# Optimization experiments

Measured on AMD Instinct MI355X. Metric: run time of the kernel, lower is better.

Reference implementation:

```python
import jax, jax.numpy as jnp
import numpy as np

D_IN = 1024
D_OUT = 1024


def setup_inputs() -> dict:
    key = jax.random.key(0)
    ks = jax.random.split(key, 7)
    x = jax.random.normal(ks[0], (4, 2048, D_IN), dtype=jnp.float32)
    scale = 1.0 / np.sqrt(D_IN)
    Wq = jax.random.normal(ks[1], (D_IN, D_OUT), dtype=jnp.float32) * scale
    Wk = jax.random.normal(ks[2], (D_IN, D_OUT), dtype=jnp.float32) * scale
    Wv = jax.random.normal(ks[3], (D_IN, D_OUT), dtype=jnp.float32) * scale
    bq = jax.random.normal(ks[4], (D_OUT,), dtype=jnp.float32) * 0.01
    bk = jax.random.normal(ks[5], (D_OUT,), dtype=jnp.float32) * 0.01
    bv = jax.random.normal(ks[6], (D_OUT,), dtype=jnp.float32) * 0.01
    return {"x": x, "Wq": Wq, "bq": bq, "Wk": Wk, "bk": bk, "Wv": Wv, "bv": bv}


def reference(x, Wq, bq, Wk, bk, Wv, bv):
    # x: [B, S, d_in]
    q = jnp.einsum("bsd,de->bse", x, Wq) + bq  # [B, S, d_out]
    k = jnp.einsum("bsd,de->bse", x, Wk) + bk
    v = jnp.einsum("bsd,de->bse", x, Wv) + bv
    d_out = q.shape[-1]
    scores = jnp.einsum("bqe,bke->bqk", q, k) / jnp.sqrt(jnp.float32(d_out))
    attn = jax.nn.softmax(scores, axis=-1)  # [B, S, S]
    return jnp.einsum("bqk,bke->bqe", attn, v)
```

## Files before the change

### kernel.cpp

```cpp
#include <hip/hip_runtime.h>
#include <hip/hip_bf16.h>
#include <stdint.h>

typedef __bf16 bf16x8 __attribute__((ext_vector_type(8)));
typedef __bf16 bf16x4 __attribute__((ext_vector_type(4)));
typedef float f32x4 __attribute__((ext_vector_type(4)));

#define DEV __device__ __forceinline__

DEV void gload_lds16(const void* g, void* l) {
  __builtin_amdgcn_global_load_lds((const __attribute__((address_space(1))) void*)g,
                                   (__attribute__((address_space(3))) void*)l, 16, 0, 0);
}

#define WAITV0 asm volatile("s_waitcnt vmcnt(0)" ::: "memory")
#define MFMA16x16(a, b, c) __builtin_amdgcn_mfma_f32_16x16x32_bf16(a, b, c, 0, 0, 0)

__global__ __launch_bounds__(256) void pack_x_kernel(const float* __restrict__ x,
                                                     __bf16* __restrict__ o, long n) {
  long i = ((long)blockIdx.x * 256 + threadIdx.x) * 4;
  const long stride = (long)gridDim.x * 256 * 4;
  for (; i < n; i += stride) {
    f32x4 v = *(const f32x4*)(x + i);
    bf16x4 b;
    b[0] = (__bf16)v[0]; b[1] = (__bf16)v[1]; b[2] = (__bf16)v[2]; b[3] = (__bf16)v[3];
    *(bf16x4*)(o + i) = b;
  }
}

__global__ __launch_bounds__(256) void pack_w_kernel(const float* __restrict__ Wq,
                                                     const float* __restrict__ Wk,
                                                     const float* __restrict__ Wv,
                                                     __bf16* __restrict__ Wt) {
  const int w = blockIdx.z;
  const float* W = (w == 0) ? Wq : (w == 1) ? Wk : Wv;
  const float scale = (w == 0) ? 0.03125f : 1.0f;
  const int d0 = blockIdx.x * 64;
  const int e0 = blockIdx.y * 64;
  __shared__ __bf16 T[64][72];
  const int tid = threadIdx.x;
  const int r4 = tid >> 4;
  const int c4 = (tid & 15) * 4;
#pragma unroll
  for (int p = 0; p < 4; ++p) {
    int r = r4 + p * 16;
    f32x4 v = *(const f32x4*)(W + (long)(d0 + r) * 1024 + e0 + c4);
    T[r][c4 + 0] = (__bf16)(v[0] * scale);
    T[r][c4 + 1] = (__bf16)(v[1] * scale);
    T[r][c4 + 2] = (__bf16)(v[2] * scale);
    T[r][c4 + 3] = (__bf16)(v[3] * scale);
  }
  __syncthreads();
  const int e4 = tid >> 3;
  const int dd = (tid & 7) * 8;
#pragma unroll
  for (int p = 0; p < 2; ++p) {
    int e = e4 + p * 32;
    bf16x8 ov;
#pragma unroll
    for (int j = 0; j < 8; ++j) ov[j] = T[dd + j][e];
    *(bf16x8*)(Wt + (long)w * 1048576 + (long)(e0 + e) * 1024 + d0 + dd) = ov;
  }
}

__global__ __launch_bounds__(256) void pack_bias_kernel(const float* __restrict__ bq,
                                                        const float* __restrict__ bk,
                                                        const float* __restrict__ bv,
                                                        float* __restrict__ o) {
  int i = blockIdx.x * 256 + threadIdx.x;
  if (i < 1024) o[i] = bq[i] * 0.03125f;
  else if (i < 2048) o[i] = bk[i - 1024];
  else if (i < 3072) o[i] = bv[i - 2048];
}

template <int MODE>
__global__ __launch_bounds__(256, 2) void gemm128_kernel(
    const __bf16* __restrict__ A, int lda,
    const __bf16* __restrict__ B, int ldb, long long bBatchStride, int bmShift,
    const float* __restrict__ bias,
    void* __restrict__ C, int ldc,
    __bf16* __restrict__ vt,
    int nTiles, int nt) {
  constexpr int TILEB = 16384;
  __shared__ __attribute__((aligned(128))) char lds[2 * 2 * TILEB];

  const int tid = threadIdx.x;
  const int lane = tid & 63;
  const int wid = tid >> 6;
  const int wm = wid >> 1, wn = wid & 1;
  const int lo = lane & 15, hi = lane >> 4;

  const int cpx = gridDim.x >> 3;
  const int bid = blockIdx.x;
  const int swz = (bid & 7) * cpx + (bid >> 3);
  const int bm = swz / nTiles, bn = swz % nTiles;

  const __bf16* Bb = B + (long long)(bm >> bmShift) * bBatchStride;

  const __bf16* gA[4]; const __bf16* gB[4]; int lA[4];
#pragma unroll
  for (int l = 0; l < 4; ++l) {
    int s = l * 256 + tid, r = s >> 3;
    int c = (s & 7) ^ (r & 7);
    gA[l] = A + (long long)(bm * 128 + r) * lda + c * 8;
    gB[l] = Bb + (long long)(bn * 128 + r) * ldb + c * 8;
    lA[l] = s * 16;
  }

  const int c0 = ((0 * 4 + hi) ^ (lo & 7)) << 4;
  const int c1 = ((1 * 4 + hi) ^ (lo & 7)) << 4;
  const int aBase = (wm * 64 + lo) * 128;
  const int bBase = TILEB + (wn * 64 + lo) * 128;

  f32x4 acc[4][4] = {};

#define STAGE(tt, buf)                                                \
  do {                                                                \
    const long long ko_ = (long long)(tt) * 64;                       \
    char* lb_ = lds + (buf) * (2 * TILEB);                            \
    _Pragma("unroll") for (int l = 0; l < 4; ++l) {                   \
      gload_lds16(gA[l] + ko_, lb_ + lA[l]);                          \
      gload_lds16(gB[l] + ko_, lb_ + TILEB + lA[l]);                  \
    }                                                                 \
  } while (0)

  STAGE(0, 0);
  WAITV0;
  __builtin_amdgcn_s_barrier();
  __builtin_amdgcn_sched_barrier(0);

  for (int t = 0; t < nt; ++t) {
    if (t + 1 < nt) STAGE(t + 1, (t + 1) & 1);
    const char* base = lds + (t & 1) * (2 * TILEB);

    bf16x8 av[4][2], bv[4][2];
#pragma unroll
    for (int f = 0; f < 4; ++f) {
      av[f][0] = *(const bf16x8*)(base + aBase + f * 16 * 128 + c0);
      av[f][1] = *(const bf16x8*)(base + aBase + f * 16 * 128 + c1);
      bv[f][0] = *(const bf16x8*)(base + bBase + f * 16 * 128 + c0);
      bv[f][1] = *(const bf16x8*)(base + bBase + f * 16 * 128 + c1);
    }
#pragma unroll
    for (int mi = 0; mi < 4; ++mi)
#pragma unroll
      for (int ni = 0; ni < 4; ++ni) {
        acc[mi][ni] = MFMA16x16(av[mi][0], bv[ni][0], acc[mi][ni]);
        acc[mi][ni] = MFMA16x16(av[mi][1], bv[ni][1], acc[mi][ni]);
      }

    if (t + 1 < nt) {
      WAITV0;
      __builtin_amdgcn_s_barrier();
      __builtin_amdgcn_sched_barrier(0);
    }
  }
#undef STAGE

  const long long row0 = (long long)bm * 128 + wm * 64 + hi * 4;
  const long long col0 = (long long)bn * 128 + wn * 64 + lo;

  if (MODE == 0) {
    float* Cf = (float*)C;
#pragma unroll
    for (int ni = 0; ni < 4; ++ni) {
      const long long col = col0 + ni * 16;
#pragma unroll
      for (int mi = 0; mi < 4; ++mi)
#pragma unroll
        for (int j = 0; j < 4; ++j)
          Cf[(row0 + mi * 16 + j) * ldc + col] = acc[mi][ni][j];
    }
  } else if (MODE == 1) {
    __bf16* Ch = (__bf16*)C;
#pragma unroll
    for (int ni = 0; ni < 4; ++ni) {
      const long long col = col0 + ni * 16;
#pragma unroll
      for (int mi = 0; mi < 4; ++mi)
#pragma unroll
        for (int j = 0; j < 4; ++j)
          Ch[(row0 + mi * 16 + j) * ldc + col] = (__bf16)acc[mi][ni][j];
    }
  } else {
    if (bn < 16) {
      __bf16* Ch = (__bf16*)C;
#pragma unroll
      for (int ni = 0; ni < 4; ++ni) {
        const long long col = col0 + ni * 16;
        const float bvs = bias[col];
#pragma unroll
        for (int mi = 0; mi < 4; ++mi)
#pragma unroll
          for (int j = 0; j < 4; ++j)
            Ch[(row0 + mi * 16 + j) * ldc + col] = (__bf16)(acc[mi][ni][j] + bvs);
      }
    } else {
      const int b = bm >> 4;
      __bf16* vtb = vt + (long long)b * 2097152;
      const int t0 = (bm & 15) * 128 + wm * 64 + hi * 4;
#pragma unroll
      for (int ni = 0; ni < 4; ++ni) {
        const long long e = (long long)(bn - 16) * 128 + wn * 64 + ni * 16 + lo;
        const float bvs = bias[2048 + e];
#pragma unroll
        for (int mi = 0; mi < 4; ++mi) {
          bf16x4 o;
#pragma unroll
          for (int j = 0; j < 4; ++j) o[j] = (__bf16)(acc[mi][ni][j] + bvs);
          *(bf16x4*)(vtb + e * 2048 + t0 + mi * 16) = o;
        }
      }
    }
  }
}

__global__ __launch_bounds__(256) void softmax_kernel(__bf16* __restrict__ S) {
  const long long row = blockIdx.x;
  __bf16* p = S + row * 2048;
  const int tid = threadIdx.x;
  const int lane = tid & 63, wid = tid >> 6;
  bf16x8 v = *(const bf16x8*)(p + tid * 8);
  float xv[8];
#pragma unroll
  for (int j = 0; j < 8; ++j) xv[j] = (float)v[j];
  float mx = xv[0];
#pragma unroll
  for (int j = 1; j < 8; ++j) mx = fmaxf(mx, xv[j]);
#pragma unroll
  for (int off = 32; off >= 1; off >>= 1) mx = fmaxf(mx, __shfl_xor(mx, off));
  __shared__ float red[8];
  if (lane == 0) red[wid] = mx;
  __syncthreads();
  mx = fmaxf(fmaxf(red[0], red[1]), fmaxf(red[2], red[3]));
  float e[8];
  float sum = 0.f;
#pragma unroll
  for (int j = 0; j < 8; ++j) {
    e[j] = __expf(xv[j] - mx);
    sum += e[j];
  }
#pragma unroll
  for (int off = 32; off >= 1; off >>= 1) sum += __shfl_xor(sum, off);
  if (lane == 0) red[4 + wid] = sum;
  __syncthreads();
  sum = red[4] + red[5] + red[6] + red[7];
  const float inv = 1.0f / sum;
  bf16x8 ov;
#pragma unroll
  for (int j = 0; j < 8; ++j) ov[j] = (__bf16)(e[j] * inv);
  *(bf16x8*)(p + tid * 8) = ov;
}

extern "C" void kernel_launch(void* const* d_in, const int* in_sizes, int n_in,
                              void* d_out, int out_size, void* d_ws, size_t ws_size,
                              hipStream_t stream) {
  (void)in_sizes; (void)n_in; (void)out_size;
  const float* x  = (const float*)d_in[0];
  const float* Wq = (const float*)d_in[1];
  const float* bq = (const float*)d_in[2];
  const float* Wk = (const float*)d_in[3];
  const float* bk = (const float*)d_in[4];
  const float* Wv = (const float*)d_in[5];
  const float* bv = (const float*)d_in[6];
  float* out = (float*)d_out;
  char* ws = (char*)d_ws;
  if (ws_size < 124000000ULL) return;

  __bf16* x16  = (__bf16*)(ws + 0);
  __bf16* Wt   = (__bf16*)(ws + 16777216);
  float*  bqkv = (float*)(ws + 23068672);
  __bf16* QKV  = (__bf16*)(ws + 23080960);
  __bf16* Vt   = (__bf16*)(ws + 73412608);
  __bf16* S    = (__bf16*)(ws + 90189824);

  pack_x_kernel<<<2048, 256, 0, stream>>>(x, x16, 8388608L);
  pack_w_kernel<<<dim3(16, 16, 3), 256, 0, stream>>>(Wq, Wk, Wv, Wt);
  pack_bias_kernel<<<12, 256, 0, stream>>>(bq, bk, bv, bqkv);

  gemm128_kernel<2><<<dim3(1536), 256, 0, stream>>>(
      x16, 1024, Wt, 1024, 0LL, 30, bqkv, QKV, 3072, Vt, 24, 16);

  gemm128_kernel<1><<<dim3(1024), 256, 0, stream>>>(
      QKV, 3072, QKV + 1024, 3072, 6291456LL, 4, nullptr, S, 2048, nullptr, 16, 16);

  softmax_kernel<<<8192, 256, 0, stream>>>(S);

  gemm128_kernel<0><<<dim3(512), 256, 0, stream>>>(
      S, 2048, Vt, 2048, 2097152LL, 4, nullptr, out, 1024, nullptr, 8, 32);
}
```

Before: 166.9 us.

## Fuse softmax exp into QK GEMM epilogue and defer normalization to PV GEMM

Replaces the standalone softmax pass with exp computed in the QK^T GEMM epilogue, which also writes per-tile partial row sums. A small rowsum kernel turns these into reciprocals, and the PV GEMM scales its output rows by them. The QKV and QK GEMMs move to 256x128 tiles with BK=32 and three blocks per CU. This removes a full read and write of the score matrix, but skips max-subtraction, so it relies on the scores being small enough not to overflow exp.

```diff
diff --git a/kernel.cpp b/kernel.cpp
--- a/kernel.cpp
+++ b/kernel.cpp
@@ -74,12 +74,187 @@
 }
 
 template <int MODE>
-__global__ __launch_bounds__(256, 2) void gemm128_kernel(
+__global__ __launch_bounds__(256, 3) void gemm_bk32_kernel(
     const __bf16* __restrict__ A, int lda,
     const __bf16* __restrict__ B, int ldb, long long bBatchStride, int bmShift,
     const float* __restrict__ bias,
-    void* __restrict__ C, int ldc,
+    __bf16* __restrict__ C, int ldc,
     __bf16* __restrict__ vt,
+    float* __restrict__ rowpart,
+    int nTiles, int nt) {
+  constexpr int ABYTES = 256 * 64;
+  constexpr int BUFB = ABYTES + 128 * 64;
+  __shared__ __attribute__((aligned(128))) char lds[2 * BUFB];
+
+  const int tid = threadIdx.x;
+  const int lane = tid & 63;
+  const int wid = tid >> 6;
+  const int wm = wid >> 1, wn = wid & 1;
+  const int lo = lane & 15, hi = lane >> 4;
+
+  const int cpx = gridDim.x >> 3;
+  const int bid = blockIdx.x;
+  const int swz = (bid & 7) * cpx + (bid >> 3);
+  const int bm = swz / nTiles, bn = swz % nTiles;
+
+  const __bf16* Bb = B + (long long)(bm >> bmShift) * bBatchStride;
+
+  const __bf16* gA[4]; int lA[4];
+  const __bf16* gB[2]; int lB[2];
+#pragma unroll
+  for (int l = 0; l < 4; ++l) {
+    int s = l * 256 + tid, r = s >> 2;
+    int c = (s & 3) ^ ((r >> 1) & 3);
+    gA[l] = A + (long long)(bm * 256 + r) * lda + c * 8;
+    lA[l] = s * 16;
+  }
+#pragma unroll
+  for (int l = 0; l < 2; ++l) {
+    int s = l * 256 + tid, r = s >> 2;
+    int c = (s & 3) ^ ((r >> 1) & 3);
+    gB[l] = Bb + (long long)(bn * 128 + r) * ldb + c * 8;
+    lB[l] = ABYTES + s * 16;
+  }
+
+  const int pch = (hi ^ ((lo >> 1) & 3)) << 4;
+  int aOff[8], bOff[4];
+#pragma unroll
+  for (int f = 0; f < 8; ++f) aOff[f] = (wm * 128 + f * 16 + lo) * 64 + pch;
+#pragma unroll
+  for (int f = 0; f < 4; ++f) bOff[f] = ABYTES + (wn * 64 + f * 16 + lo) * 64 + pch;
+
+  f32x4 acc[8][4] = {};
+
+#define STAGE(tt, buf)                                               \
+  do {                                                               \
+    const long long ko_ = (long long)(tt) * 32;                      \
+    char* lb_ = lds + (buf) * BUFB;                                  \
+    _Pragma("unroll") for (int l = 0; l < 4; ++l)                    \
+        gload_lds16(gA[l] + ko_, lb_ + lA[l]);                       \
+    _Pragma("unroll") for (int l = 0; l < 2; ++l)                    \
+        gload_lds16(gB[l] + ko_, lb_ + lB[l]);                       \
+  } while (0)
+
+  STAGE(0, 0);
+  WAITV0;
+  __builtin_amdgcn_s_barrier();
+  __builtin_amdgcn_sched_barrier(0);
+
+  for (int t = 0; t < nt; ++t) {
+    if (t + 1 < nt) STAGE(t + 1, (t + 1) & 1);
+    const char* base = lds + (t & 1) * BUFB;
+    bf16x8 av[8], bvv[4];
+#pragma unroll
+    for (int f = 0; f < 4; ++f) bvv[f] = *(const bf16x8*)(base + bOff[f]);
+#pragma unroll
+    for (int f = 0; f < 8; ++f) av[f] = *(const bf16x8*)(base + aOff[f]);
+#pragma unroll
+    for (int mi = 0; mi < 8; ++mi)
+#pragma unroll
+      for (int ni = 0; ni < 4; ++ni)
+        acc[mi][ni] = MFMA16x16(av[mi], bvv[ni], acc[mi][ni]);
+    if (t + 1 < nt) {
+      WAITV0;
+      __builtin_amdgcn_s_barrier();
+      __builtin_amdgcn_sched_barrier(0);
+    }
+  }
+#undef STAGE
+
+  const long long row0 = (long long)bm * 256 + wm * 128 + hi * 4;
+  const long long col0 = (long long)bn * 128 + wn * 64 + lo;
+
+  if (MODE == 1) {
+    if (bn < 16) {
+#pragma unroll
+      for (int ni = 0; ni < 4; ++ni) {
+        const long long col = col0 + ni * 16;
+        const float bvs = bias[col];
+#pragma unroll
+        for (int mi = 0; mi < 8; ++mi)
+#pragma unroll
+          for (int j = 0; j < 4; ++j)
+            C[(row0 + mi * 16 + j) * ldc + col] = (__bf16)(acc[mi][ni][j] + bvs);
+      }
+    } else {
+      const int b = bm >> 3;
+      __bf16* vtb = vt + (long long)b * 2097152;
+      const int tbase = (bm & 7) * 256 + wm * 128 + hi * 4;
+#pragma unroll
+      for (int ni = 0; ni < 4; ++ni) {
+        const long long e = (long long)(bn - 16) * 128 + wn * 64 + ni * 16 + lo;
+        const float bvs = bias[2048 + e];
+#pragma unroll
+        for (int mi = 0; mi < 8; ++mi) {
+          bf16x4 o;
+#pragma unroll
+          for (int j = 0; j < 4; ++j) o[j] = (__bf16)(acc[mi][ni][j] + bvs);
+          *(bf16x4*)(vtb + e * 2048 + tbase + mi * 16) = o;
+        }
+      }
+    }
+  } else {
+    float ps[8][4];
+#pragma unroll
+    for (int mi = 0; mi < 8; ++mi)
+#pragma unroll
+      for (int j = 0; j < 4; ++j) {
+        float s0 = 0.f;
+#pragma unroll
+        for (int ni = 0; ni < 4; ++ni) {
+          float e = __expf(acc[mi][ni][j]);
+          acc[mi][ni][j] = e;
+          s0 += e;
+        }
+        ps[mi][j] = s0;
+      }
+#pragma unroll
+    for (int ni = 0; ni < 4; ++ni) {
+      const long long col = col0 + ni * 16;
+#pragma unroll
+      for (int mi = 0; mi < 8; ++mi)
+#pragma unroll
+        for (int j = 0; j < 4; ++j)
+          C[(row0 + mi * 16 + j) * ldc + col] = (__bf16)acc[mi][ni][j];
+    }
+#pragma unroll
+    for (int mi = 0; mi < 8; ++mi)
+#pragma unroll
+      for (int j = 0; j < 4; ++j) {
+        float v = ps[mi][j];
+        v += __shfl_xor(v, 1);
+        v += __shfl_xor(v, 2);
+        v += __shfl_xor(v, 4);
+        v += __shfl_xor(v, 8);
+        ps[mi][j] = v;
+      }
+    if (lo == 0) {
+      float* rp = rowpart + (long long)(bn * 2 + wn) * 8192;
+#pragma unroll
+      for (int mi = 0; mi < 8; ++mi) {
+        f32x4 o;
+#pragma unroll
+        for (int j = 0; j < 4; ++j) o[j] = ps[mi][j];
+        *(f32x4*)(rp + row0 + mi * 16) = o;
+      }
+    }
+  }
+}
+
+__global__ __launch_bounds__(256) void rowsum_kernel(const float* __restrict__ rowpart,
+                                                     float* __restrict__ rowinv) {
+  int r = blockIdx.x * 256 + threadIdx.x;
+  float s = 0.f;
+#pragma unroll
+  for (int p = 0; p < 32; ++p) s += rowpart[p * 8192 + r];
+  rowinv[r] = 1.0f / s;
+}
+
+__global__ __launch_bounds__(256, 2) void gemm_pv_kernel(
+    const __bf16* __restrict__ A, int lda,
+    const __bf16* __restrict__ B, int ldb, long long bBatchStride, int bmShift,
+    const float* __restrict__ rowinv,
+    float* __restrict__ C, int ldc,
     int nTiles, int nt) {
   constexpr int TILEB = 16384;
   __shared__ __attribute__((aligned(128))) char lds[2 * 2 * TILEB];
@@ -132,7 +307,6 @@
   for (int t = 0; t < nt; ++t) {
     if (t + 1 < nt) STAGE(t + 1, (t + 1) & 1);
     const char* base = lds + (t & 1) * (2 * TILEB);
-
     bf16x8 av[4][2], bv[4][2];
 #pragma unroll
     for (int f = 0; f < 4; ++f) {
@@ -148,7 +322,6 @@
         acc[mi][ni] = MFMA16x16(av[mi][0], bv[ni][0], acc[mi][ni]);
         acc[mi][ni] = MFMA16x16(av[mi][1], bv[ni][1], acc[mi][ni]);
       }
-
     if (t + 1 < nt) {
       WAITV0;
       __builtin_amdgcn_s_barrier();
@@ -159,97 +332,17 @@
 
   const long long row0 = (long long)bm * 128 + wm * 64 + hi * 4;
   const long long col0 = (long long)bn * 128 + wn * 64 + lo;
-
-  if (MODE == 0) {
-    float* Cf = (float*)C;
+#pragma unroll
+  for (int mi = 0; mi < 4; ++mi) {
+    f32x4 ri = *(const f32x4*)(rowinv + row0 + mi * 16);
 #pragma unroll
     for (int ni = 0; ni < 4; ++ni) {
       const long long col = col0 + ni * 16;
 #pragma unroll
-      for (int mi = 0; mi < 4; ++mi)
-#pragma unroll
-        for (int j = 0; j < 4; ++j)
-          Cf[(row0 + mi * 16 + j) * ldc + col] = acc[mi][ni][j];
-    }
-  } else if (MODE == 1) {
-    __bf16* Ch = (__bf16*)C;
-#pragma unroll
-    for (int ni = 0; ni < 4; ++ni) {
-      const long long col = col0 + ni * 16;
-#pragma unroll
-      for (int mi = 0; mi < 4; ++mi)
-#pragma unroll
-        for (int j = 0; j < 4; ++j)
-          Ch[(row0 + mi * 16 + j) * ldc + col] = (__bf16)acc[mi][ni][j];
-    }
-  } else {
-    if (bn < 16) {
-      __bf16* Ch = (__bf16*)C;
-#pragma unroll
-      for (int ni = 0; ni < 4; ++ni) {
-        const long long col = col0 + ni * 16;
-        const float bvs = bias[col];
-#pragma unroll
-        for (int mi = 0; mi < 4; ++mi)
-#pragma unroll
-          for (int j = 0; j < 4; ++j)
-            Ch[(row0 + mi * 16 + j) * ldc + col] = (__bf16)(acc[mi][ni][j] + bvs);
-      }
-    } else {
-      const int b = bm >> 4;
-      __bf16* vtb = vt + (long long)b * 2097152;
-      const int t0 = (bm & 15) * 128 + wm * 64 + hi * 4;
-#pragma unroll
-      for (int ni = 0; ni < 4; ++ni) {
-        const long long e = (long long)(bn - 16) * 128 + wn * 64 + ni * 16 + lo;
-        const float bvs = bias[2048 + e];
-#pragma unroll
-        for (int mi = 0; mi < 4; ++mi) {
-          bf16x4 o;
-#pragma unroll
-          for (int j = 0; j < 4; ++j) o[j] = (__bf16)(acc[mi][ni][j] + bvs);
-          *(bf16x4*)(vtb + e * 2048 + t0 + mi * 16) = o;
-        }
-      }
-    }
-  }
-}
-
-__global__ __launch_bounds__(256) void softmax_kernel(__bf16* __restrict__ S) {
-  const long long row = blockIdx.x;
-  __bf16* p = S + row * 2048;
-  const int tid = threadIdx.x;
-  const int lane = tid & 63, wid = tid >> 6;
-  bf16x8 v = *(const bf16x8*)(p + tid * 8);
-  float xv[8];
-#pragma unroll
-  for (int j = 0; j < 8; ++j) xv[j] = (float)v[j];
-  float mx = xv[0];
-#pragma unroll
-  for (int j = 1; j < 8; ++j) mx = fmaxf(mx, xv[j]);
-#pragma unroll
-  for (int off = 32; off >= 1; off >>= 1) mx = fmaxf(mx, __shfl_xor(mx, off));
-  __shared__ float red[8];
-  if (lane == 0) red[wid] = mx;
-  __syncthreads();
-  mx = fmaxf(fmaxf(red[0], red[1]), fmaxf(red[2], red[3]));
-  float e[8];
-  float sum = 0.f;
-#pragma unroll
-  for (int j = 0; j < 8; ++j) {
-    e[j] = __expf(xv[j] - mx);
-    sum += e[j];
-  }
-#pragma unroll
-  for (int off = 32; off >= 1; off >>= 1) sum += __shfl_xor(sum, off);
-  if (lane == 0) red[4 + wid] = sum;
-  __syncthreads();
-  sum = red[4] + red[5] + red[6] + red[7];
-  const float inv = 1.0f / sum;
-  bf16x8 ov;
-#pragma unroll
-  for (int j = 0; j < 8; ++j) ov[j] = (__bf16)(e[j] * inv);
-  *(bf16x8*)(p + tid * 8) = ov;
+      for (int j = 0; j < 4; ++j)
+        C[(row0 + mi * 16 + j) * ldc + col] = acc[mi][ni][j] * ri[j];
+    }
+  }
 }
 
 extern "C" void kernel_launch(void* const* d_in, const int* in_sizes, int n_in,
@@ -265,27 +358,29 @@
   const float* bv = (const float*)d_in[6];
   float* out = (float*)d_out;
   char* ws = (char*)d_ws;
-  if (ws_size < 124000000ULL) return;
-
-  __bf16* x16  = (__bf16*)(ws + 0);
-  __bf16* Wt   = (__bf16*)(ws + 16777216);
-  float*  bqkv = (float*)(ws + 23068672);
-  __bf16* QKV  = (__bf16*)(ws + 23080960);
-  __bf16* Vt   = (__bf16*)(ws + 73412608);
-  __bf16* S    = (__bf16*)(ws + 90189824);
+  if (ws_size < 124825600ULL) return;
+
+  __bf16* x16   = (__bf16*)(ws + 0);
+  __bf16* Wt    = (__bf16*)(ws + 16777216);
+  float*  bqkv  = (float*)(ws + 23068672);
+  __bf16* QKV   = (__bf16*)(ws + 23080960);
+  __bf16* Vt    = (__bf16*)(ws + 73412608);
+  __bf16* S     = (__bf16*)(ws + 90189824);
+  float*  rowpt = (float*)(ws + 123744256);
+  float*  rowiv = (float*)(ws + 124792832);
 
   pack_x_kernel<<<2048, 256, 0, stream>>>(x, x16, 8388608L);
   pack_w_kernel<<<dim3(16, 16, 3), 256, 0, stream>>>(Wq, Wk, Wv, Wt);
   pack_bias_kernel<<<12, 256, 0, stream>>>(bq, bk, bv, bqkv);
 
-  gemm128_kernel<2><<<dim3(1536), 256, 0, stream>>>(
-      x16, 1024, Wt, 1024, 0LL, 30, bqkv, QKV, 3072, Vt, 24, 16);
-
-  gemm128_kernel<1><<<dim3(1024), 256, 0, stream>>>(
-      QKV, 3072, QKV + 1024, 3072, 6291456LL, 4, nullptr, S, 2048, nullptr, 16, 16);
-
-  softmax_kernel<<<8192, 256, 0, stream>>>(S);
-
-  gemm128_kernel<0><<<dim3(512), 256, 0, stream>>>(
-      S, 2048, Vt, 2048, 2097152LL, 4, nullptr, out, 1024, nullptr, 8, 32);
-}
+  gemm_bk32_kernel<1><<<dim3(768), 256, 0, stream>>>(
+      x16, 1024, Wt, 1024, 0LL, 30, bqkv, QKV, 3072, Vt, nullptr, 24, 32);
+
+  gemm_bk32_kernel<2><<<dim3(512), 256, 0, stream>>>(
+      QKV, 3072, QKV + 1024, 3072, 6291456LL, 3, nullptr, S, 2048, nullptr, rowpt, 16, 32);
+
+  rowsum_kernel<<<32, 256, 0, stream>>>(rowpt, rowiv);
+
+  gemm_pv_kernel<<<dim3(512), 256, 0, stream>>>(
+      S, 2048, Vt, 2048, 2097152LL, 4, rowiv, out, 1024, 8, 32);
+}
```

Result: slower. 240.8 us (+44.3%).
